# Optimization experiments

Hardware: AMD Instinct MI355X
Metric: run time of the kernel (lower is better)

The kernel has to match this reference:

```python
import jax, jax.numpy as jnp
import numpy as np

D = 1024
ITERATIONS = 2


def setup_inputs() -> dict:
    key = jax.random.key(0)
    ks = jax.random.split(key, 7)
    s = 1.0 / np.sqrt(D)  # PyTorch GRUCell/Linear init scale
    x = jax.random.normal(ks[0], (8, 4096, D), dtype=jnp.float32)
    W_ih = jax.random.uniform(ks[1], (3 * D, D), minval=-s, maxval=s, dtype=jnp.float32)
    W_hh = jax.random.uniform(ks[2], (3 * D, D), minval=-s, maxval=s, dtype=jnp.float32)
    b_ih = jax.random.uniform(ks[3], (3 * D,), minval=-s, maxval=s, dtype=jnp.float32)
    b_hh = jax.random.uniform(ks[4], (3 * D,), minval=-s, maxval=s, dtype=jnp.float32)
    We = jax.random.uniform(ks[5], (1, D), minval=-s, maxval=s, dtype=jnp.float32)
    be = jax.random.uniform(ks[6], (1,), minval=-s, maxval=s, dtype=jnp.float32)
    return {"x": x, "W_ih": W_ih, "W_hh": W_hh, "b_ih": b_ih, "b_hh": b_hh, "We": We, "be": be}


def _gru_cell(inp, h, W_ih, W_hh, b_ih, b_hh):
    # PyTorch GRUCell gate order: r, z, n
    gi = inp @ W_ih.T + b_ih  # [N, 3D]
    gh = h @ W_hh.T + b_hh    # [N, 3D]
    i_r, i_z, i_n = jnp.split(gi, 3, axis=-1)
    h_r, h_z, h_n = jnp.split(gh, 3, axis=-1)
    r = jax.nn.sigmoid(i_r + h_r)
    z = jax.nn.sigmoid(i_z + h_z)
    n = jnp.tanh(i_n + r * h_n)
    return (1.0 - z) * n + z * h


def reference(x, W_ih, W_hh, b_ih, b_hh, We, be):
    B, S, Dm = x.shape
    state = x.reshape(-1, Dm)  # [B*S, D]
    for _ in range(ITERATIONS):
        error = jax.nn.sigmoid(state @ We.T + be)  # [B*S, 1]
        new_state = _gru_cell(state, state, W_ih, W_hh, b_ih, b_hh)
        state = (1.0 - error) * state + error * new_state
    return state.reshape(B, S, Dm)
```

## Files before the change

### kernel.cpp

```cpp
#include <hip/hip_runtime.h>

#define DD 1024

typedef int   i32x4  __attribute__((ext_vector_type(4)));
typedef int   i32x8  __attribute__((ext_vector_type(8)));
typedef float f32x4  __attribute__((ext_vector_type(4)));

__device__ __forceinline__ float sigm(float x) { return 1.0f / (1.0f + __expf(-x)); }
__device__ __forceinline__ float tanh_fast(float x) {
  float e = __expf(-2.0f * fabsf(x));
  float t = (1.0f - e) / (1.0f + e);
  return copysignf(t, x);
}
__device__ __forceinline__ void gload_lds16(const void* g, void* l) {
  __builtin_amdgcn_global_load_lds((const __attribute__((address_space(1))) void*)g,
                                   (__attribute__((address_space(3))) void*)l, 16, 0, 0);
}
__device__ __forceinline__ unsigned pk_fp8x4(float a, float b, float c, float d) {
  int u = __builtin_amdgcn_cvt_pk_fp8_f32(a, b, 0, false);
  u = __builtin_amdgcn_cvt_pk_fp8_f32(c, d, u, true);
  return (unsigned)u;
}

__global__ __launch_bounds__(256) void prep_weights(
    const float* __restrict__ Wih, const float* __restrict__ Whh,
    const float* __restrict__ bih, const float* __restrict__ bhh,
    unsigned char* __restrict__ Wcat8, float* __restrict__ bias) {
  int i = blockIdx.x * 256 + threadIdx.x;
  int g = i >> 18;
  int rem = i & 262143;
  int n = rem >> 8;
  int k4 = rem & 255;
  const float4* wih4 = reinterpret_cast<const float4*>(Wih);
  const float4* whh4 = reinterpret_cast<const float4*>(Whh);
  float4 v;
  if (g == 0) {
    size_t idx = (size_t)n * 256 + k4;
    float4 a = wih4[idx], b = whh4[idx];
    v = make_float4(a.x + b.x, a.y + b.y, a.z + b.z, a.w + b.w);
  } else if (g == 1) {
    size_t idx = (size_t)(DD + n) * 256 + k4;
    float4 a = wih4[idx], b = whh4[idx];
    v = make_float4(a.x + b.x, a.y + b.y, a.z + b.z, a.w + b.w);
  } else if (g == 2) {
    size_t idx = (size_t)(2 * DD + n) * 256 + k4;
    v = wih4[idx];
  } else {
    size_t idx = (size_t)(2 * DD + n) * 256 + k4;
    v = whh4[idx];
  }
  reinterpret_cast<unsigned*>(Wcat8)[i] =
      pk_fp8x4(v.x * 32.0f, v.y * 32.0f, v.z * 32.0f, v.w * 32.0f);

  if (i < 4 * DD) {
    int bg = i >> 10, bn = i & 1023;
    float bv;
    if (bg == 0)      bv = bih[bn] + bhh[bn];
    else if (bg == 1) bv = bih[DD + bn] + bhh[DD + bn];
    else if (bg == 2) bv = bih[2 * DD + bn];
    else              bv = bhh[2 * DD + bn];
    bias[i] = bv;
  }
}

__global__ __launch_bounds__(256) void error_cast(
    const float* S, const float* __restrict__ We, const float* __restrict__ be,
    unsigned char* __restrict__ Sb8, float* __restrict__ err) {
  __shared__ float part[4];
  const int row = blockIdx.x;
  const int t = threadIdx.x;
  float4 v = reinterpret_cast<const float4*>(S + (size_t)row * DD)[t];
  float4 w = reinterpret_cast<const float4*>(We)[t];
  float dot = v.x * w.x + v.y * w.y + v.z * w.z + v.w * w.w;
  reinterpret_cast<unsigned*>(Sb8 + (size_t)row * DD)[t] = pk_fp8x4(v.x, v.y, v.z, v.w);
#pragma unroll
  for (int off = 32; off > 0; off >>= 1) dot += __shfl_xor(dot, off);
  if ((t & 63) == 0) part[t >> 6] = dot;
  __syncthreads();
  if (t == 0) err[row] = sigm(part[0] + part[1] + part[2] + part[3] + be[0]);
}

__global__ __launch_bounds__(256, 2) void gru_fused_gemm(
    const unsigned char* __restrict__ Sb8,
    const unsigned char* __restrict__ Wcat8,
    const float* __restrict__ bias,
    const float* __restrict__ err,
    const float* Sf,
    float* out, int M) {
  __shared__ alignas(16) unsigned char As[2 * 16384];
  __shared__ alignas(16) unsigned char Bs[2 * 16384];

  const int nwg = gridDim.x;
  const int bid = blockIdx.x;
  const int swz = (bid & 7) * (nwg >> 3) + (bid >> 3);
  const int db = swz & 31;
  const int rb = swz >> 5;

  const int tid = threadIdx.x;
  const int w = tid >> 6;
  const int lane = tid & 63;
  const int l15 = lane & 15;
  const int q = lane >> 4;
  const int wr = w >> 1, wc = w & 1;

  const int l8r = lane >> 3;
  const int glog = (lane & 7) ^ l8r;
  const unsigned char* srcA[4];
  const unsigned char* srcB[4];
  unsigned char* dstA[4];
  unsigned char* dstB[4];
#pragma unroll
  for (int i = 0; i < 4; ++i) {
    int j = w + i * 4;
    int row = j * 8 + l8r;
    srcA[i] = Sb8 + (size_t)(rb * 128 + row) * DD + glog * 16;
    int gate = (row >> 4) & 3;
    int dgl = (row & 15) + (row >> 6) * 16;
    srcB[i] = Wcat8 + (size_t)(gate * DD + db * 32 + dgl) * DD + glog * 16;
    dstA[i] = As + j * 1024;
    dstB[i] = Bs + j * 1024;
  }

  const int lx = lane & 7;
  const int s0 = ((2 * q) ^ lx) * 16;
  const int s1 = ((2 * q + 1) ^ lx) * 16;
  int abase[4], bbase[4];
#pragma unroll
  for (int mi = 0; mi < 4; ++mi) abase[mi] = (wr * 64 + mi * 16 + l15) * 128;
#pragma unroll
  for (int g = 0; g < 4; ++g)   bbase[g] = (wc * 64 + g * 16 + l15) * 128;

  f32x4 acc[4][4];
#pragma unroll
  for (int mi = 0; mi < 4; ++mi)
#pragma unroll
    for (int g = 0; g < 4; ++g) acc[mi][g] = f32x4{0.f, 0.f, 0.f, 0.f};

  auto stage = [&](int t) {
    const int slot = (t & 1) * 16384;
    const int koff = t * 128;
#pragma unroll
    for (int i = 0; i < 4; ++i) {
      gload_lds16(srcA[i] + koff, dstA[i] + slot);
      gload_lds16(srcB[i] + koff, dstB[i] + slot);
    }
  };

  stage(0);
  stage(1);

  for (int t = 0; t < 8; ++t) {
    const int sb = (t & 1) * 16384;
    if (t < 7) asm volatile("s_waitcnt vmcnt(8)" ::: "memory");
    else       asm volatile("s_waitcnt vmcnt(0)" ::: "memory");
    __builtin_amdgcn_s_barrier();

    const unsigned char* Ab = As + sb;
    const unsigned char* Bb = Bs + sb;
    i32x8 a[4], b[4];
#pragma unroll
    for (int mi = 0; mi < 4; ++mi) {
      i32x4 a0 = *reinterpret_cast<const i32x4*>(Ab + abase[mi] + s0);
      i32x4 a1 = *reinterpret_cast<const i32x4*>(Ab + abase[mi] + s1);
      a[mi] = __builtin_shufflevector(a0, a1, 0, 1, 2, 3, 4, 5, 6, 7);
    }
#pragma unroll
    for (int g = 0; g < 4; ++g) {
      i32x4 b0 = *reinterpret_cast<const i32x4*>(Bb + bbase[g] + s0);
      i32x4 b1 = *reinterpret_cast<const i32x4*>(Bb + bbase[g] + s1);
      b[g] = __builtin_shufflevector(b0, b1, 0, 1, 2, 3, 4, 5, 6, 7);
    }
    asm volatile("s_waitcnt lgkmcnt(0)" ::: "memory");
    __builtin_amdgcn_s_barrier();

    if (t <= 5) stage(t + 2);

    __builtin_amdgcn_s_setprio(1);
#pragma unroll
    for (int g = 0; g < 4; ++g)
#pragma unroll
      for (int mi = 0; mi < 4; ++mi)
        acc[mi][g] = __builtin_amdgcn_mfma_scale_f32_16x16x128_f8f6f4(
            a[mi], b[g], acc[mi][g], 0, 0, 0, 0x7F7F7F7F, 0, 0x7A7A7A7A);
    __builtin_amdgcn_s_setprio(0);
  }

  const int dgcol = db * 32 + wc * 16 + l15;
  const float b_r = bias[dgcol];
  const float b_z = bias[DD + dgcol];
  const float b_i = bias[2 * DD + dgcol];
  const float b_h = bias[3 * DD + dgcol];
#pragma unroll
  for (int mi = 0; mi < 4; ++mi) {
#pragma unroll
    for (int j = 0; j < 4; ++j) {
      int m = rb * 128 + wr * 64 + mi * 16 + q * 4 + j;
      float e = err[m];
      float hh = Sf[(size_t)m * DD + dgcol];
      float r = sigm(acc[mi][0][j] + b_r);
      float z = sigm(acc[mi][1][j] + b_z);
      float n = tanh_fast(acc[mi][2][j] + b_i + r * (acc[mi][3][j] + b_h));
      out[(size_t)m * DD + dgcol] = hh + e * (1.0f - z) * (n - hh);
    }
  }
}

extern "C" void kernel_launch(void* const* d_in, const int* in_sizes, int n_in,
                              void* d_out, int out_size, void* d_ws, size_t ws_size,
                              hipStream_t stream) {
  const float* x   = (const float*)d_in[0];
  const float* Wih = (const float*)d_in[1];
  const float* Whh = (const float*)d_in[2];
  const float* bih = (const float*)d_in[3];
  const float* bhh = (const float*)d_in[4];
  const float* We  = (const float*)d_in[5];
  const float* be  = (const float*)d_in[6];
  float* out = (float*)d_out;
  const int M = in_sizes[0] / DD;

  char* ws = (char*)d_ws;
  unsigned char* Sb8   = (unsigned char*)ws;
  unsigned char* Wcat8 = (unsigned char*)(ws + (size_t)M * DD);
  float* bias = (float*)(ws + (size_t)M * DD + (size_t)4 * DD * DD);
  float* err  = (float*)(ws + (size_t)M * DD + (size_t)4 * DD * DD + (size_t)4 * DD * 4);

  prep_weights<<<4096, 256, 0, stream>>>(Wih, Whh, bih, bhh, Wcat8, bias);

  const int nwg = (M / 128) * 32;
  const float* S = x;
  for (int it = 0; it < 2; ++it) {
    error_cast<<<M, 256, 0, stream>>>(S, We, be, Sb8, err);
    gru_fused_gemm<<<nwg, 256, 0, stream>>>(Sb8, Wcat8, bias, err, S, out, M);
    S = out;
  }
}
```

Before: 515.9 us.

## Transpose LDS tile layout and remap workgroup swizzle to fixed 2x4 grouping

Changes the global-to-LDS staging so each 8-lane group loads 8 different rows at the same k-chunk, which stores tiles in a k-chunk-major layout instead of the row-major XOR-swizzled one. The fragment reads use matching new base offsets. This is meant to remove bank conflicts without XOR address arithmetic. The workgroup-to-tile mapping is also changed to a fixed split of 8 XCD-style groups over 2 column halves and 4 row quarters, which aims at L2 reuse of A and B tiles. The new mapping hardcodes 32 column blocks and 256 row blocks, so it only holds for M=32768, and global loads become less coalesced per row.

```diff
diff --git a/kernel.cpp b/kernel.cpp
--- a/kernel.cpp
+++ b/kernel.cpp
@@ -90,11 +90,11 @@
   __shared__ alignas(16) unsigned char As[2 * 16384];
   __shared__ alignas(16) unsigned char Bs[2 * 16384];
 
-  const int nwg = gridDim.x;
   const int bid = blockIdx.x;
-  const int swz = (bid & 7) * (nwg >> 3) + (bid >> 3);
-  const int db = swz & 31;
-  const int rb = swz >> 5;
+  const int x = bid & 7;
+  const int c = bid >> 3;
+  const int db = (x & 1) * 16 + (c & 15);
+  const int rb = (x >> 1) * 64 + (c >> 4);
 
   const int tid = threadIdx.x;
   const int w = tid >> 6;
@@ -103,8 +103,8 @@
   const int q = lane >> 4;
   const int wr = w >> 1, wc = w & 1;
 
-  const int l8r = lane >> 3;
-  const int glog = (lane & 7) ^ l8r;
+  const int r7 = lane & 7;
+  const int gp = lane >> 3;
   const unsigned char* srcA[4];
   const unsigned char* srcB[4];
   unsigned char* dstA[4];
@@ -112,23 +112,17 @@
 #pragma unroll
   for (int i = 0; i < 4; ++i) {
     int j = w + i * 4;
-    int row = j * 8 + l8r;
-    srcA[i] = Sb8 + (size_t)(rb * 128 + row) * DD + glog * 16;
+    int row = j * 8 + r7;
+    srcA[i] = Sb8 + (size_t)(rb * 128 + row) * DD + gp * 16;
     int gate = (row >> 4) & 3;
     int dgl = (row & 15) + (row >> 6) * 16;
-    srcB[i] = Wcat8 + (size_t)(gate * DD + db * 32 + dgl) * DD + glog * 16;
+    srcB[i] = Wcat8 + (size_t)(gate * DD + db * 32 + dgl) * DD + gp * 16;
     dstA[i] = As + j * 1024;
     dstB[i] = Bs + j * 1024;
   }
 
-  const int lx = lane & 7;
-  const int s0 = ((2 * q) ^ lx) * 16;
-  const int s1 = ((2 * q + 1) ^ lx) * 16;
-  int abase[4], bbase[4];
-#pragma unroll
-  for (int mi = 0; mi < 4; ++mi) abase[mi] = (wr * 64 + mi * 16 + l15) * 128;
-#pragma unroll
-  for (int g = 0; g < 4; ++g)   bbase[g] = (wc * 64 + g * 16 + l15) * 128;
+  const int abase = (wr * 8 + (l15 >> 3)) * 1024 + 2 * q * 128 + (l15 & 7) * 16;
+  const int bbase = (wc * 8 + (l15 >> 3)) * 1024 + 2 * q * 128 + (l15 & 7) * 16;
 
   f32x4 acc[4][4];
 #pragma unroll
@@ -160,14 +154,14 @@
     i32x8 a[4], b[4];
 #pragma unroll
     for (int mi = 0; mi < 4; ++mi) {
-      i32x4 a0 = *reinterpret_cast<const i32x4*>(Ab + abase[mi] + s0);
-      i32x4 a1 = *reinterpret_cast<const i32x4*>(Ab + abase[mi] + s1);
+      i32x4 a0 = *reinterpret_cast<const i32x4*>(Ab + abase + mi * 2048);
+      i32x4 a1 = *reinterpret_cast<const i32x4*>(Ab + abase + mi * 2048 + 128);
       a[mi] = __builtin_shufflevector(a0, a1, 0, 1, 2, 3, 4, 5, 6, 7);
     }
 #pragma unroll
     for (int g = 0; g < 4; ++g) {
-      i32x4 b0 = *reinterpret_cast<const i32x4*>(Bb + bbase[g] + s0);
-      i32x4 b1 = *reinterpret_cast<const i32x4*>(Bb + bbase[g] + s1);
+      i32x4 b0 = *reinterpret_cast<const i32x4*>(Bb + bbase + g * 2048);
+      i32x4 b1 = *reinterpret_cast<const i32x4*>(Bb + bbase + g * 2048 + 128);
       b[g] = __builtin_shufflevector(b0, b1, 0, 1, 2, 3, 4, 5, 6, 7);
     }
     asm volatile("s_waitcnt lgkmcnt(0)" ::: "memory");
```

Measured after the change: 715.7 us. 1.39x slower.
